# Kernel optimization log

Hardware: AMD Instinct MI355X
Metric: run time of the kernel (lower is better)

The kernel has to match this reference:

```python
import jax, jax.numpy as jnp
import numpy as np

B, T, D, M = 32, 2048, 128, 256   # batch, seq_len, pitch vocab d, encoder_output_dim m
FILTERS = [256, 256, 256]
TAU = 1.0                          # gumbel_temperature
ALPHA_INV = 1.0 / (D * 100)        # W init value: 1/alpha, alpha = d*100


def causal_dilated_conv(x, w, b, dilation):
    """x: [B,T,Cin], w: [K,Cin,Cout], causal left padding."""
    k = w.shape[0]
    pad = (k - 1) * dilation
    y = jax.lax.conv_general_dilated(
        x, w, window_strides=(1,), padding=[(pad, 0)],
        rhs_dilation=(dilation,),
        dimension_numbers=('NWC', 'WIO', 'NWC'))
    return y + b


def slow_weight_model(batch, w0, b0, w1, b1, w2, b2, w_out, b_out):
    """DilatedConvBlock: stack of causal dilated convs (relu) + 1x1 readout to m logits."""
    h = jax.nn.relu(causal_dilated_conv(batch, w0, b0, dilation=1))
    h = jax.nn.relu(causal_dilated_conv(h, w1, b1, dilation=2))
    h = jax.nn.relu(causal_dilated_conv(h, w2, b2, dilation=4))
    return causal_dilated_conv(h, w_out, b_out, dilation=1)  # [B,T,M] logits


def setup_inputs() -> dict:
    key = jax.random.key(0)
    ks = jax.random.split(key, 9)
    def glorot(k, shape):
        fan_in = np.prod(shape[:-1])
        return (jax.random.normal(k, shape, jnp.float32) / np.sqrt(fan_in)).astype(jnp.float32)
    return {
        'batch': jax.random.uniform(ks[0], (B, T, D), jnp.float32),
        'w0': glorot(ks[1], (2, D, FILTERS[0])), 'b0': jnp.zeros((FILTERS[0],), jnp.float32),
        'w1': glorot(ks[2], (2, FILTERS[0], FILTERS[1])), 'b1': jnp.zeros((FILTERS[1],), jnp.float32),
        'w2': glorot(ks[3], (2, FILTERS[1], FILTERS[2])), 'b2': jnp.zeros((FILTERS[2],), jnp.float32),
        'w_out': glorot(ks[4], (1, FILTERS[2], M)), 'b_out': jnp.zeros((M,), jnp.float32),
    }


def reference(batch, w0, b0, w1, b1, w2, b2, w_out, b_out):
    logits = slow_weight_model(batch, w0, b0, w1, b1, w2, b2, w_out, b_out)  # [B,T,M]
    # short_term_method == 'softmax_normalize_after'
    h_src = jax.nn.softmax(logits / TAU, axis=2)  # [B,T,M]
    s_tar = batch                                  # [B,T,D]
    W0 = jnp.full((B, M, D), ALPHA_INV, jnp.float32)

    def step(W, hs):
        h, s = hs                                              # [B,M], [B,D]
        num = jnp.einsum('bm,bmd->bd', h, W)                   # readout
        prob = num / jnp.sum(num, axis=-1, keepdims=True)      # normalize-after
        W_new = W + h[:, :, None] * s[:, None, :]              # outer-product fast-weight update
        return W_new, prob

    W_final, probs = jax.lax.scan(
        step, W0, (jnp.swapaxes(h_src, 0, 1), jnp.swapaxes(s_tar, 0, 1)))
    probs = jnp.swapaxes(probs, 0, 1)  # [B,T,D]
    return probs, W_final
```

## Files before the change

kernel.cpp:

```cpp
#include <hip/hip_runtime.h>

using u16 = unsigned short;
using u32 = unsigned int;
using short8 = __attribute__((ext_vector_type(8))) short;
using short4v = __attribute__((ext_vector_type(4))) short;
using bf16x8 = __attribute__((ext_vector_type(8))) __bf16;
using f32x4 = __attribute__((ext_vector_type(4))) float;

#define ALPHA_INV (1.0f / (128.0f * 100.0f))

__device__ __forceinline__ u32 swz(u32 off, u32 row) { return off ^ ((row & 7u) << 4); }

__device__ __forceinline__ u16 f2bf(float x) {
  u32 u = __float_as_uint(x);
  u32 r = u + 0x7fffu + ((u >> 16) & 1u);
  return (u16)(r >> 16);
}

__device__ __forceinline__ float bf2f(u16 x) {
  u32 u = ((u32)x) << 16;
  return __uint_as_float(u);
}

__device__ __forceinline__ f32x4 mfma(bf16x8 a, bf16x8 b, f32x4 c) {
  return __builtin_amdgcn_mfma_f32_16x16x32_bf16(a, b, c, 0, 0, 0);
}

__global__ void wtrans(const float* __restrict__ w, u16* __restrict__ o, int rows, int cin) {
  int idx = blockIdx.x * 256 + threadIdx.x;
  if (idx >= rows * 256) return;
  int row = idx >> 8, n = idx & 255;
  int tap = row / cin, c = row - tap * cin;
  o[((size_t)tap * 256 + n) * cin + c] = f2bf(w[idx]);
}

__global__ void cvt_bf16_kernel(const float* __restrict__ in, u16* __restrict__ out) {
  int i = blockIdx.x * 256 + threadIdx.x;
  float4 v = ((const float4*)in)[i];
  short4v o;
  o[0] = (short)f2bf(v.x); o[1] = (short)f2bf(v.y);
  o[2] = (short)f2bf(v.z); o[3] = (short)f2bf(v.w);
  *(short4v*)(out + (size_t)i * 4) = o;
}

__global__ __launch_bounds__(256) void transpose_s(const u16* __restrict__ S,
                                                   u16* __restrict__ ST) {
  __shared__ u16 L[64 * 129];
  const int tid = threadIdx.x;
  const int t0 = blockIdx.x * 64;
  const int b = blockIdx.y;
  const u16* src = S + ((size_t)b * 2048 + t0) * 128;
#pragma unroll
  for (int it = 0; it < 4; ++it) {
    int s = tid + it * 256;
    int t = s >> 4, c8 = s & 15;
    short8 v = *(const short8*)(src + t * 128 + c8 * 8);
#pragma unroll
    for (int j = 0; j < 8; ++j) L[t * 129 + c8 * 8 + j] = (u16)v[j];
  }
  __syncthreads();
  u16* dst = ST + (size_t)b * 128 * 2048 + t0;
#pragma unroll
  for (int it = 0; it < 4; ++it) {
    int s = tid + it * 256;
    int oct = s & 7, d = s >> 3;
    short8 v;
#pragma unroll
    for (int j = 0; j < 8; ++j) v[j] = (short)L[(oct * 8 + j) * 129 + d];
    *(short8*)(dst + (size_t)d * 2048 + oct * 8) = v;
  }
}

template <int CIN, int DIL, int TAPS, bool RELU, bool SOFTMAX>
__global__ __launch_bounds__(512) void conv_kernel(
    const u16* __restrict__ in, const u16* __restrict__ wt,
    const float* __restrict__ bias, u16* __restrict__ out) {
  constexpr int BM = 128, BN = 256, BK = 64;
  __shared__ alignas(16) u16 Al[BM * BK];
  __shared__ alignas(16) u16 Bl[BN * BK];
  __shared__ float redA[4][BM];
  __shared__ float redB[4][BM];

  const int tid = threadIdx.x;
  const int wid = tid >> 6, lane = tid & 63;
  const int wr = wid >> 2, wc = wid & 3;
  const int lg = lane >> 4, lq = lane & 15;
  const int row0 = blockIdx.x * BM;
  const int tloc0 = row0 & 2047;

  f32x4 acc[4][4];
#pragma unroll
  for (int i = 0; i < 4; ++i)
#pragma unroll
    for (int j = 0; j < 4; ++j) acc[i][j] = (f32x4)0.0f;

#pragma unroll
  for (int tap = 0; tap < TAPS; ++tap) {
    const int shift = (TAPS - 1 - tap) * DIL;
#pragma unroll
    for (int kc = 0; kc < CIN / BK; ++kc) {
#pragma unroll
      for (int it = 0; it < 2; ++it) {
        int s = tid + it * 512;
        int r = s >> 3, cb = s & 7;
        short8 v = (short8)0;
        if (tloc0 + r >= shift)
          v = *(const short8*)(in + (size_t)(row0 + r - shift) * CIN + kc * BK + cb * 8);
        *(short8*)((char*)Al + swz(r * 128 + cb * 16, r)) = v;
      }
#pragma unroll
      for (int it = 0; it < 4; ++it) {
        int s = tid + it * 512;
        int n = s >> 3, cb = s & 7;
        *(short8*)((char*)Bl + swz(n * 128 + cb * 16, n)) =
            *(const short8*)(wt + ((size_t)tap * BN + n) * CIN + kc * BK + cb * 8);
      }
      __syncthreads();
#pragma unroll
      for (int ks = 0; ks < 2; ++ks) {
        bf16x8 af[4], bfr[4];
#pragma unroll
        for (int mi = 0; mi < 4; ++mi) {
          int r = wr * 64 + mi * 16 + lq;
          af[mi] = *(const bf16x8*)((const char*)Al + swz(r * 128 + ks * 64 + lg * 16, r));
        }
#pragma unroll
        for (int ni = 0; ni < 4; ++ni) {
          int n = wc * 64 + ni * 16 + lq;
          bfr[ni] = *(const bf16x8*)((const char*)Bl + swz(n * 128 + ks * 64 + lg * 16, n));
        }
#pragma unroll
        for (int mi = 0; mi < 4; ++mi)
#pragma unroll
          for (int ni = 0; ni < 4; ++ni)
            acc[mi][ni] = mfma(af[mi], bfr[ni], acc[mi][ni]);
      }
      __syncthreads();
    }
  }

  float bcol[4];
#pragma unroll
  for (int ni = 0; ni < 4; ++ni) bcol[ni] = bias[wc * 64 + ni * 16 + lq];
#pragma unroll
  for (int mi = 0; mi < 4; ++mi)
#pragma unroll
    for (int ni = 0; ni < 4; ++ni)
#pragma unroll
      for (int rr = 0; rr < 4; ++rr) acc[mi][ni][rr] += bcol[ni];

  if constexpr (!SOFTMAX) {
#pragma unroll
    for (int mi = 0; mi < 4; ++mi)
#pragma unroll
      for (int ni = 0; ni < 4; ++ni)
#pragma unroll
        for (int rr = 0; rr < 4; ++rr) {
          float v = acc[mi][ni][rr];
          if (RELU) v = fmaxf(v, 0.0f);
          int row = row0 + wr * 64 + mi * 16 + lg * 4 + rr;
          int col = wc * 64 + ni * 16 + lq;
          out[(size_t)row * BN + col] = f2bf(v);
        }
  } else {
    float tmx[4][4];
#pragma unroll
    for (int mi = 0; mi < 4; ++mi)
#pragma unroll
      for (int rr = 0; rr < 4; ++rr) {
        float v = fmaxf(fmaxf(acc[mi][0][rr], acc[mi][1][rr]),
                        fmaxf(acc[mi][2][rr], acc[mi][3][rr]));
#pragma unroll
        for (int off = 1; off < 16; off <<= 1) v = fmaxf(v, __shfl_xor(v, off));
        if (lq == 0) redA[wc][wr * 64 + mi * 16 + lg * 4 + rr] = v;
      }
    __syncthreads();
#pragma unroll
    for (int mi = 0; mi < 4; ++mi)
#pragma unroll
      for (int rr = 0; rr < 4; ++rr) {
        int rb = wr * 64 + mi * 16 + lg * 4 + rr;
        tmx[mi][rr] = fmaxf(fmaxf(redA[0][rb], redA[1][rb]),
                            fmaxf(redA[2][rb], redA[3][rb]));
      }
#pragma unroll
    for (int mi = 0; mi < 4; ++mi)
#pragma unroll
      for (int rr = 0; rr < 4; ++rr) {
        float s = 0.0f;
#pragma unroll
        for (int ni = 0; ni < 4; ++ni) {
          float p = __expf(acc[mi][ni][rr] - tmx[mi][rr]);
          acc[mi][ni][rr] = p;
          s += p;
        }
#pragma unroll
        for (int off = 1; off < 16; off <<= 1) s += __shfl_xor(s, off);
        if (lq == 0) redB[wc][wr * 64 + mi * 16 + lg * 4 + rr] = s;
      }
    __syncthreads();
#pragma unroll
    for (int mi = 0; mi < 4; ++mi)
#pragma unroll
      for (int rr = 0; rr < 4; ++rr) {
        int rb = wr * 64 + mi * 16 + lg * 4 + rr;
        float inv = 1.0f / (redB[0][rb] + redB[1][rb] + redB[2][rb] + redB[3][rb]);
        int row = row0 + rb;
#pragma unroll
        for (int ni = 0; ni < 4; ++ni) {
          int col = wc * 64 + ni * 16 + lq;
          out[(size_t)row * BN + col] = f2bf(acc[mi][ni][rr] * inv);
        }
      }
  }
}

__global__ __launch_bounds__(512) void gchunk(
    const u16* __restrict__ H, const u16* __restrict__ ST,
    u16* __restrict__ G0, u16* __restrict__ G1) {
  constexpr int M = 256, T = 2048;
  __shared__ alignas(16) u16 Hl[128 * 128];
  __shared__ alignas(16) u16 Sl[128 * 128];
  const int tid = threadIdx.x;
  const int wid = tid >> 6, lane = tid & 63;
  const int dg = wid >> 2, mg = wid & 3;
  const int lg = lane >> 4, lq = lane & 15;
  const int b = blockIdx.x, mh = blockIdx.y, j = blockIdx.z;
  u16* G = (mh == 0 ? G0 : G1);

#pragma unroll
  for (int it = 0; it < 4; ++it) {
    int s = tid + it * 512;
    int t = s >> 4, c8 = s & 15;
    *(short8*)((char*)Hl + swz(t * 256 + c8 * 16, t)) =
        *(const short8*)(H + ((size_t)b * T + j * 128 + t) * M + mh * 128 + c8 * 8);
  }
#pragma unroll
  for (int it = 0; it < 4; ++it) {
    int s = tid + it * 512;
    int d = s >> 4, c8 = s & 15;
    *(short8*)((char*)Sl + swz(d * 256 + c8 * 16, d)) =
        *(const short8*)(ST + ((size_t)b * 128 + d) * T + j * 128 + c8 * 8);
  }
  __syncthreads();

  f32x4 acc[4][2];
#pragma unroll
  for (int di = 0; di < 4; ++di)
#pragma unroll
    for (int mi = 0; mi < 2; ++mi) acc[di][mi] = (f32x4)0.0f;

#pragma unroll
  for (int ks = 0; ks < 4; ++ks) {
    bf16x8 sfrag[4];
#pragma unroll
    for (int di = 0; di < 4; ++di) {
      int d = dg * 64 + di * 16 + lq;
      sfrag[di] = *(const bf16x8*)((const char*)Sl + swz(d * 256 + ks * 64 + lg * 16, d));
    }
#pragma unroll
    for (int mi = 0; mi < 2; ++mi) {
      int ml = mg * 32 + mi * 16 + lq;
      short8 hr;
#pragma unroll
      for (int jj = 0; jj < 8; ++jj) {
        int t = ks * 32 + lg * 8 + jj;
        hr[jj] = (short)*(const u16*)((const char*)Hl + swz(t * 256 + ml * 2, t));
      }
      bf16x8 hfrag = __builtin_bit_cast(bf16x8, hr);
#pragma unroll
      for (int di = 0; di < 4; ++di) acc[di][mi] = mfma(sfrag[di], hfrag, acc[di][mi]);
    }
  }

  u16* Gj = G + (((size_t)b * 16 + j) << 14);
#pragma unroll
  for (int di = 0; di < 4; ++di)
#pragma unroll
    for (int mi = 0; mi < 2; ++mi)
#pragma unroll
      for (int rr = 0; rr < 4; ++rr) {
        int d = dg * 64 + di * 16 + lg * 4 + rr;
        int ml = mg * 32 + mi * 16 + lq;
        Gj[d * 128 + ml] = f2bf(acc[di][mi][rr]);
      }
}

__global__ __launch_bounds__(256) void prefix_scan(
    u16* __restrict__ G0, u16* __restrict__ G1, float* __restrict__ Wtmp) {
  u16* G = blockIdx.y ? G1 : G0;
  float* W = Wtmp + (size_t)blockIdx.y * (32 * 128 * 128);
  int idx = blockIdx.x * 256 + threadIdx.x;
  int mo = idx & 15, d = (idx >> 4) & 127, b = idx >> 11;
  size_t base = (((size_t)b * 16) * 128 + d) * 128 + mo * 8;
  float acc[8];
#pragma unroll
  for (int k = 0; k < 8; ++k) acc[k] = ALPHA_INV;
  for (int j = 0; j < 16; ++j) {
    u16* p = G + base + (size_t)j * 16384;
    short8 g = *(short8*)p;
    short8 c;
#pragma unroll
    for (int k = 0; k < 8; ++k) c[k] = (short)f2bf(acc[k]);
    *(short8*)p = c;
#pragma unroll
    for (int k = 0; k < 8; ++k) acc[k] += bf2f((u16)g[k]);
  }
  float* w = W + ((size_t)b * 128 + d) * 128 + mo * 8;
  *(float4*)w = make_float4(acc[0], acc[1], acc[2], acc[3]);
  *(float4*)(w + 4) = make_float4(acc[4], acc[5], acc[6], acc[7]);
}

__global__ __launch_bounds__(256) void wfin_t(const float* __restrict__ Wtmp,
                                              float* __restrict__ wfin) {
  __shared__ float L[128 * 129];
  const int tid = threadIdx.x;
  const int b = blockIdx.x, h = blockIdx.y;
  const float* src = Wtmp + (size_t)h * (32 * 128 * 128) + (size_t)b * 16384;
#pragma unroll
  for (int it = 0; it < 16; ++it) {
    int idx = tid + it * 256;
    int d = idx >> 5, q = idx & 31;
    *(float4*)&L[d * 129 + q * 4] = *(const float4*)&src[d * 128 + q * 4];
  }
  __syncthreads();
  float* dst = wfin + (size_t)b * 32768 + (size_t)h * 16384;
#pragma unroll
  for (int it = 0; it < 16; ++it) {
    int idx = tid + it * 256;
    int ml = idx >> 5, dq = idx & 31;
    float4 v;
    v.x = L[(dq * 4 + 0) * 129 + ml];
    v.y = L[(dq * 4 + 1) * 129 + ml];
    v.z = L[(dq * 4 + 2) * 129 + ml];
    v.w = L[(dq * 4 + 3) * 129 + ml];
    *(float4*)&dst[ml * 128 + dq * 4] = v;
  }
}

__global__ __launch_bounds__(512) void attn_chunk(
    const u16* __restrict__ H, const u16* __restrict__ ST,
    const u16* __restrict__ C0, const u16* __restrict__ C1,
    float* __restrict__ out) {
  constexpr int M = 256, D = 128, T = 2048;
  __shared__ alignas(16) u16 Hi[128 * 256];
  __shared__ alignas(16) u16 Sl[128 * 128];
  __shared__ alignas(16) u16 Ct[128 * 128];

  const int tid = threadIdx.x;
  const int wid = tid >> 6, lane = tid & 63;
  const int lg = lane >> 4, lq = lane & 15;
  const int b = blockIdx.x, i = blockIdx.y;
  const size_t hrow0 = (size_t)b * T + i * 128;

  bf16x8 aq[8];
  {
    const u16* qrow = H + (hrow0 + wid * 16 + lq) * M;
#pragma unroll
    for (int ks = 0; ks < 8; ++ks) aq[ks] = *(const bf16x8*)(qrow + ks * 32 + lg * 8);
  }

#pragma unroll
  for (int it = 0; it < 8; ++it) {
    int s = tid + it * 512;
    int r = s >> 5, c = s & 31;
    *(short8*)((char*)Hi + swz(r * 512 + c * 16, r)) =
        *(const short8*)(H + (hrow0 + r) * M + c * 8);
  }
#pragma unroll
  for (int it = 0; it < 4; ++it) {
    int s = tid + it * 512;
    int d = s >> 4, c8 = s & 15;
    *(short8*)((char*)Sl + swz(d * 256 + c8 * 16, d)) =
        *(const short8*)(ST + ((size_t)b * D + d) * T + i * 128 + c8 * 8);
  }
  const size_t coff = ((size_t)b * 16 + i) * (128 * 128);
#pragma unroll
  for (int it = 0; it < 4; ++it) {
    int s = tid + it * 512;
    int d = s >> 4, c8 = s & 15;
    *(short8*)((char*)Ct + swz(d * 256 + c8 * 16, d)) = *(const short8*)(C0 + coff + d * 128 + c8 * 8);
  }
  __syncthreads();

  f32x4 accO[8];
#pragma unroll
  for (int df = 0; df < 8; ++df) accO[df] = (f32x4)0.0f;

#pragma unroll
  for (int ks = 0; ks < 4; ++ks)
#pragma unroll
    for (int df = 0; df < 8; ++df) {
      int d = df * 16 + lq;
      bf16x8 bf = *(const bf16x8*)((const char*)Ct + swz(d * 256 + ks * 64 + lg * 16, d));
      accO[df] = mfma(aq[ks], bf, accO[df]);
    }
  __syncthreads();
#pragma unroll
  for (int it = 0; it < 4; ++it) {
    int s = tid + it * 512;
    int d = s >> 4, c8 = s & 15;
    *(short8*)((char*)Ct + swz(d * 256 + c8 * 16, d)) = *(const short8*)(C1 + coff + d * 128 + c8 * 8);
  }
  __syncthreads();
#pragma unroll
  for (int ks = 0; ks < 4; ++ks)
#pragma unroll
    for (int df = 0; df < 8; ++df) {
      int d = df * 16 + lq;
      bf16x8 bf = *(const bf16x8*)((const char*)Ct + swz(d * 256 + ks * 64 + lg * 16, d));
      accO[df] = mfma(aq[4 + ks], bf, accO[df]);
    }
  __syncthreads();

  f32x4 accP[8];
#pragma unroll
  for (int cf = 0; cf < 8; ++cf) accP[cf] = (f32x4)0.0f;
#pragma unroll
  for (int ks = 0; ks < 8; ++ks)
#pragma unroll
    for (int cf = 0; cf < 8; ++cf) {
      int tt = cf * 16 + lq;
      bf16x8 bf = *(const bf16x8*)((const char*)Hi + swz(tt * 512 + ks * 64 + lg * 16, tt));
      accP[cf] = mfma(aq[ks], bf, accP[cf]);
    }
  char* Pw = (char*)Ct + wid * 4096;
#pragma unroll
  for (int cf = 0; cf < 8; ++cf)
#pragma unroll
    for (int rr = 0; rr < 4; ++rr) {
      int ql = lg * 4 + rr;
      int tl = cf * 16 + lq;
      float v = accP[cf][rr];
      if (tl >= wid * 16 + ql) v = 0.0f;
      *(u16*)(Pw + swz(ql * 256 + tl * 2, ql)) = f2bf(v);
    }
#pragma unroll
  for (int ks = 0; ks < 4; ++ks) {
    bf16x8 a = *(const bf16x8*)(Pw + swz(lq * 256 + ks * 64 + lg * 16, lq));
#pragma unroll
    for (int df = 0; df < 8; ++df) {
      int d = df * 16 + lq;
      bf16x8 bf = *(const bf16x8*)((const char*)Sl + swz(d * 256 + ks * 64 + lg * 16, d));
      accO[df] = mfma(a, bf, accO[df]);
    }
  }

#pragma unroll
  for (int rr = 0; rr < 4; ++rr) {
    float ssum = 0.0f;
#pragma unroll
    for (int df = 0; df < 8; ++df) ssum += accO[df][rr];
#pragma unroll
    for (int off = 1; off < 16; off <<= 1) ssum += __shfl_xor(ssum, off);
    float inv = 1.0f / ssum;
    size_t row = hrow0 + wid * 16 + lg * 4 + rr;
#pragma unroll
    for (int df = 0; df < 8; ++df)
      out[row * D + df * 16 + lq] = accO[df][rr] * inv;
  }
}

extern "C" void kernel_launch(void* const* d_in, const int* in_sizes, int n_in,
                              void* d_out, int out_size, void* d_ws, size_t ws_size,
                              hipStream_t stream) {
  const float* batch = (const float*)d_in[0];
  const float* w0 = (const float*)d_in[1];
  const float* b0 = (const float*)d_in[2];
  const float* w1 = (const float*)d_in[3];
  const float* b1 = (const float*)d_in[4];
  const float* w2 = (const float*)d_in[5];
  const float* b2 = (const float*)d_in[6];
  const float* wo = (const float*)d_in[7];
  const float* bo = (const float*)d_in[8];

  const size_t SZ_S = 16777216;
  const size_t SZ_BUF = 33554432;
  const size_t NEED = SZ_S + 2 * SZ_BUF + 786432;
  if (ws_size < NEED) return;

  char* ws = (char*)d_ws;
  u16* S = (u16*)ws;
  u16* bufA = (u16*)(ws + SZ_S);
  u16* bufB = (u16*)(ws + SZ_S + SZ_BUF);
  u16* Wt0 = (u16*)(ws + SZ_S + 2 * SZ_BUF);
  u16* Wt1 = Wt0 + 2 * 256 * 128;
  u16* Wt2 = Wt1 + 2 * 256 * 256;
  u16* Wt3 = Wt2 + 2 * 256 * 256;
  u16* ST = bufA;
  u16* G0 = (u16*)ws;
  u16* G1 = (u16*)(ws + 2 * SZ_S);
  float* probs = (float*)d_out;
  float* wfin = probs + (size_t)32 * 2048 * 128;
  float* Wtmp = probs;

  wtrans<<<256, 256, 0, stream>>>(w0, Wt0, 2 * 128, 128);
  wtrans<<<512, 256, 0, stream>>>(w1, Wt1, 2 * 256, 256);
  wtrans<<<512, 256, 0, stream>>>(w2, Wt2, 2 * 256, 256);
  wtrans<<<256, 256, 0, stream>>>(wo, Wt3, 1 * 256, 256);
  cvt_bf16_kernel<<<8192, 256, 0, stream>>>(batch, S);

  conv_kernel<128, 1, 2, true, false><<<512, 512, 0, stream>>>(S, Wt0, b0, bufA);
  conv_kernel<256, 2, 2, true, false><<<512, 512, 0, stream>>>(bufA, Wt1, b1, bufB);
  conv_kernel<256, 4, 2, true, false><<<512, 512, 0, stream>>>(bufB, Wt2, b2, bufA);
  conv_kernel<256, 1, 1, false, true><<<512, 512, 0, stream>>>(bufA, Wt3, bo, bufB);

  transpose_s<<<dim3(32, 32), 256, 0, stream>>>(S, ST);
  gchunk<<<dim3(32, 2, 16), 512, 0, stream>>>(bufB, ST, G0, G1);
  prefix_scan<<<dim3(256, 2), 256, 0, stream>>>(G0, G1, Wtmp);
  wfin_t<<<dim3(32, 2), 256, 0, stream>>>(Wtmp, wfin);
  attn_chunk<<<dim3(32, 16), 512, 0, stream>>>(bufB, ST, G0, G1, probs);
}
```

Baseline: 202.6 us.

## Pre-swizzle activations and weights in global memory; load tiles via global_load_lds

Producers (weight transpose, input conversion, conv epilogue) now write bf16 data in a pre-XOR-swizzled layout within each 64-element slice. The conv kernel can then copy A and B tiles straight into LDS with direct global-to-LDS loads instead of staging them through registers. Fragment reads apply a row-shift-adjusted swizzle key, and the causal-padding boundary tiles fall back to register loads. This removes the VGPR round trip and the separate LDS stores, at the cost of coupling every producer and consumer to the swizzled layout, which could silently break correctness if any of them disagree.

```diff
diff --git a/kernel.cpp b/kernel.cpp
--- a/kernel.cpp
+++ b/kernel.cpp
@@ -26,12 +26,20 @@
   return __builtin_amdgcn_mfma_f32_16x16x32_bf16(a, b, c, 0, 0, 0);
 }
 
+__device__ __forceinline__ void gl16(const void* g, void* l) {
+  __builtin_amdgcn_global_load_lds(
+      (const __attribute__((address_space(1))) unsigned int*)g,
+      (__attribute__((address_space(3))) unsigned int*)l, 16, 0, 0);
+}
+
 __global__ void wtrans(const float* __restrict__ w, u16* __restrict__ o, int rows, int cin) {
   int idx = blockIdx.x * 256 + threadIdx.x;
   if (idx >= rows * 256) return;
   int row = idx >> 8, n = idx & 255;
   int tap = row / cin, c = row - tap * cin;
-  o[((size_t)tap * 256 + n) * cin + c] = f2bf(w[idx]);
+  int kc = c >> 6, ci = c & 63;
+  u32 sb = (u32)(ci * 2) ^ ((u32)(n & 7) << 4);
+  o[((size_t)tap * 256 + n) * cin + kc * 64 + (sb >> 1)] = f2bf(w[idx]);
 }
 
 __global__ void cvt_bf16_kernel(const float* __restrict__ in, u16* __restrict__ out) {
@@ -40,7 +48,11 @@
   short4v o;
   o[0] = (short)f2bf(v.x); o[1] = (short)f2bf(v.y);
   o[2] = (short)f2bf(v.z); o[3] = (short)f2bf(v.w);
-  *(short4v*)(out + (size_t)i * 4) = o;
+  int e = i * 4;
+  int row = e >> 7, c = e & 127;
+  int slice = c >> 6, ci = c & 63;
+  u32 sb = (u32)(ci * 2) ^ ((u32)(row & 7) << 4);
+  *(short4v*)(out + (size_t)row * 128 + slice * 64 + (sb >> 1)) = o;
 }
 
 __global__ __launch_bounds__(256) void transpose_s(const u16* __restrict__ S,
@@ -54,7 +66,9 @@
   for (int it = 0; it < 4; ++it) {
     int s = tid + it * 256;
     int t = s >> 4, c8 = s & 15;
-    short8 v = *(const short8*)(src + t * 128 + c8 * 8);
+    int slice = c8 >> 3;
+    u32 sb = (u32)((c8 & 7) * 16) ^ ((u32)(t & 7) << 4);
+    short8 v = *(const short8*)(src + t * 128 + slice * 64 + (sb >> 1));
 #pragma unroll
     for (int j = 0; j < 8; ++j) L[t * 129 + c8 * 8 + j] = (u16)v[j];
   }
@@ -99,21 +113,33 @@
     const int shift = (TAPS - 1 - tap) * DIL;
 #pragma unroll
     for (int kc = 0; kc < CIN / BK; ++kc) {
-#pragma unroll
-      for (int it = 0; it < 2; ++it) {
-        int s = tid + it * 512;
-        int r = s >> 3, cb = s & 7;
-        short8 v = (short8)0;
-        if (tloc0 + r >= shift)
-          v = *(const short8*)(in + (size_t)(row0 + r - shift) * CIN + kc * BK + cb * 8);
-        *(short8*)((char*)Al + swz(r * 128 + cb * 16, r)) = v;
-      }
-#pragma unroll
-      for (int it = 0; it < 4; ++it) {
-        int s = tid + it * 512;
-        int n = s >> 3, cb = s & 7;
-        *(short8*)((char*)Bl + swz(n * 128 + cb * 16, n)) =
-            *(const short8*)(wt + ((size_t)tap * BN + n) * CIN + kc * BK + cb * 8);
+      if (shift > 0 && tloc0 == 0) {
+#pragma unroll
+        for (int it = 0; it < 2; ++it) {
+          int gi = tid + it * 512;
+          int r = gi >> 3, cg = gi & 7;
+          short8 v = (short8)0;
+          if (r >= shift)
+            v = *(const short8*)(in + (size_t)(row0 + r - shift) * CIN + kc * BK + cg * 8);
+          *(short8*)((char*)Al + gi * 16) = v;
+        }
+      } else {
+#pragma unroll
+        for (int it = 0; it < 2; ++it) {
+          int gi = tid + it * 512;
+          int r = gi >> 3, cg = gi & 7;
+          gl16(in + (size_t)(row0 + r - shift) * CIN + kc * BK + cg * 8,
+               (char*)Al + it * 8192 + wid * 1024);
+        }
+      }
+      {
+        const u16* wtb = wt + ((size_t)(tap * 256)) * CIN + kc * BK;
+#pragma unroll
+        for (int it = 0; it < 4; ++it) {
+          int gi = tid + it * 512;
+          int n = gi >> 3, cg = gi & 7;
+          gl16(wtb + (size_t)n * CIN + cg * 8, (char*)Bl + it * 8192 + wid * 1024);
+        }
       }
       __syncthreads();
 #pragma unroll
@@ -122,7 +148,8 @@
 #pragma unroll
         for (int mi = 0; mi < 4; ++mi) {
           int r = wr * 64 + mi * 16 + lq;
-          af[mi] = *(const bf16x8*)((const char*)Al + swz(r * 128 + ks * 64 + lg * 16, r));
+          af[mi] = *(const bf16x8*)((const char*)Al +
+                                    swz(r * 128 + ks * 64 + lg * 16, (u32)(r - shift + 8)));
         }
 #pragma unroll
         for (int ni = 0; ni < 4; ++ni) {
@@ -160,7 +187,9 @@
           if (RELU) v = fmaxf(v, 0.0f);
           int row = row0 + wr * 64 + mi * 16 + lg * 4 + rr;
           int col = wc * 64 + ni * 16 + lq;
-          out[(size_t)row * BN + col] = f2bf(v);
+          int ci = col & 63;
+          u32 sb = (u32)(ci * 2) ^ ((u32)(row & 7) << 4);
+          out[(size_t)row * BN + wc * 64 + (sb >> 1)] = f2bf(v);
         }
   } else {
     float tmx[4][4];
```

New measurement: 204.8 us. About the same (+1.1%).
